# Kernel optimization log

Measured on AMD Instinct MI355X. Metric: run time of the kernel, lower is better.

Reference implementation:

```python
import jax, jax.numpy as jnp
import numpy as np

MARGIN = 0.5
SCALE = 64.0

N, D, C, S = 512, 512, 100000, 1


def setup_inputs() -> dict:
    key = jax.random.key(0)
    k1, k2, k3 = jax.random.split(key, 3)
    emb = jax.random.normal(k1, (N, D), dtype=jnp.float32)
    # Real face pipelines feed L2-normalized embeddings; also keeps acos well-conditioned.
    emb = emb / jnp.linalg.norm(emb, axis=1, keepdims=True)
    w = jax.random.normal(k2, (D, C, S), dtype=jnp.float32)
    labels = jax.random.randint(k3, (N,), 0, C)
    target = jax.nn.one_hot(labels, C, dtype=jnp.float32)  # [N, C]
    return {"embedding_batch": emb, "w_param": w, "target_batch": target}


def reference(embedding_batch, w_param, target_batch):
    # normalize class centers over the embedding dim (dim=0 of w)
    w_n = w_param / jnp.linalg.norm(w_param, axis=0, keepdims=True)  # [D, C, S]
    # cosine similarities via GEMM instead of broadcast mult-reduce: [N, C, S]
    cos = jnp.einsum('nd,dcs->ncs', embedding_batch, w_n)
    cos = jnp.clip(cos, -1.0, 1.0)
    cos = jnp.max(cos, axis=2)                    # best subclass -> [N, C]
    theta = jnp.arccos(cos)                       # [N, C]
    logits = jnp.cos(theta + target_batch * MARGIN) * SCALE
    # faithful to the original: softmax over dim=0 (the batch axis)
    return jax.nn.softmax(logits, axis=0)
```

## Files before the change

### kernel.cpp

```cpp
#include <hip/hip_runtime.h>
#include <hip/hip_bf16.h>


static constexpr int DIM    = 512;
static constexpr int NROWS  = 512;
static constexpr int NCLS   = 100000;
static constexpr int BC     = 32;
static constexpr int BK     = 32;
static constexpr int NSTEP  = DIM / BK;
static constexpr int MT     = NROWS / 16;
static constexpr int NBLK   = NCLS / BC;

static constexpr float COS_M = 0.87758256189037271611f;
static constexpr float SIN_M = 0.47942553860420300027f;
static constexpr float SCALE = 64.0f;
static constexpr float SHIFT = 20.0f;

typedef __attribute__((ext_vector_type(8))) short bf16x8;
typedef __attribute__((ext_vector_type(4))) float f32x4;

#define MFMA16(A, B, C) __builtin_amdgcn_mfma_f32_16x16x32_bf16((A), (B), (C), 0, 0, 0)

__device__ __forceinline__ unsigned short f2bf(float f) {
  union { float f; unsigned u; } v; v.f = f;
  unsigned u = v.u;
  return (unsigned short)((u + 0x7FFFu + ((u >> 16) & 1u)) >> 16);
}

__global__ __launch_bounds__(1024)
void label_scan(const float* __restrict__ tgt, int* __restrict__ labels) {
  const int row = blockIdx.x;
  const int nq = NCLS / 4;
  const int q0 = blockIdx.y * (nq / 4);
  const int q1 = (blockIdx.y == 3) ? nq : q0 + (nq / 4);
  const float4* rp = reinterpret_cast<const float4*>(tgt + (size_t)row * NCLS);
  int found = -1;
  for (int c4 = q0 + threadIdx.x; c4 < q1; c4 += 1024) {
    const float4 v = rp[c4];
    if (v.x > 0.5f) found = c4 * 4 + 0;
    if (v.y > 0.5f) found = c4 * 4 + 1;
    if (v.z > 0.5f) found = c4 * 4 + 2;
    if (v.w > 0.5f) found = c4 * 4 + 3;
  }
  if (found >= 0) labels[row] = found;
}

__global__ void prep_afrag(const float* __restrict__ emb,
                           unsigned short* __restrict__ afrag) {
  const int idx = blockIdx.x * blockDim.x + threadIdx.x;
  const int l  = idx & 63;
  const int mt = (idx >> 6) & 31;
  const int ks = idx >> 11;
  const int row = mt * 16 + (l & 15);
  const int k0  = ks * 32 + (l >> 4) * 8;

  unsigned short t[8];
#pragma unroll
  for (int j = 0; j < 8; ++j) t[j] = f2bf(emb[row * DIM + k0 + j]);

  uint4 v;
  v.x = (unsigned)t[0] | ((unsigned)t[1] << 16);
  v.y = (unsigned)t[2] | ((unsigned)t[3] << 16);
  v.z = (unsigned)t[4] | ((unsigned)t[5] << 16);
  v.w = (unsigned)t[6] | ((unsigned)t[7] << 16);
  *reinterpret_cast<uint4*>(&afrag[(size_t)idx * 8]) = v;
}

__global__ __launch_bounds__(256)
void wt_kernel(const float* __restrict__ w,
               unsigned short* __restrict__ bfrag,
               float* __restrict__ rnorm) {
  __shared__ float S[32][33];
  __shared__ float NRM[32][32];

  const int t  = threadIdx.x;
  const int cb = blockIdx.x;
  const int c0 = cb * 32;

  const int rk = t >> 3;
  const int rc = (t & 7) * 4;

  float4 nrm4 = {0.f, 0.f, 0.f, 0.f};

  for (int p = 0; p < NSTEP; ++p) {
    const float4 v = *reinterpret_cast<const float4*>(
        w + (size_t)(p * BK + rk) * NCLS + c0 + rc);
    nrm4.x += v.x * v.x; nrm4.y += v.y * v.y;
    nrm4.z += v.z * v.z; nrm4.w += v.w * v.w;
    __syncthreads();
    *reinterpret_cast<float4*>(&S[rk][rc]) = v;
    __syncthreads();

    if (t < 128) {
      const int l2 = t & 63;
      const int j  = t >> 6;
      const int col = j * 16 + (l2 & 15);
      const int kb  = (l2 >> 4) * 8;
      uint4 pk;
      pk.x = (unsigned)f2bf(S[kb + 0][col]) | ((unsigned)f2bf(S[kb + 1][col]) << 16);
      pk.y = (unsigned)f2bf(S[kb + 2][col]) | ((unsigned)f2bf(S[kb + 3][col]) << 16);
      pk.z = (unsigned)f2bf(S[kb + 4][col]) | ((unsigned)f2bf(S[kb + 5][col]) << 16);
      pk.w = (unsigned)f2bf(S[kb + 6][col]) | ((unsigned)f2bf(S[kb + 7][col]) << 16);
      *reinterpret_cast<uint4*>(
          &bfrag[(((size_t)(cb * NSTEP + p) * 2 + j) * 64 + l2) * 8]) = pk;
    }
  }

  NRM[rk][rc + 0] = nrm4.x;
  NRM[rk][rc + 1] = nrm4.y;
  NRM[rk][rc + 2] = nrm4.z;
  NRM[rk][rc + 3] = nrm4.w;
  __syncthreads();
  if (t < 32) {
    float s = 0.f;
#pragma unroll
    for (int g = 0; g < 32; ++g) s += NRM[g][t];
    rnorm[c0 + t] = rsqrtf(fmaxf(s, 1e-20f));
  }
}

__global__ __launch_bounds__(1024, 8)
void arcface_main(const unsigned short* __restrict__ bfrag,
                  const unsigned short* __restrict__ afrag,
                  const float* __restrict__ rnorm,
                  const int* __restrict__ labels,
                  float* __restrict__ out) {
  __shared__ alignas(16) unsigned short B3[3][1024];
  __shared__ float red[16][BC];
  __shared__ float colv[BC];

  const int tid = threadIdx.x;
  const int wv  = tid >> 6;
  const int l   = tid & 63;
  const int lh  = l >> 4;
  const int ll  = l & 15;
  const int c0  = blockIdx.x * BC;

  const char* bfb  = (const char*)bfrag + (size_t)blockIdx.x * 32768;
  const char* aptr = (const char*)afrag + (size_t)(wv * 2) * 1024 + (size_t)l * 16;
  char* b3b = (char*)&B3[0][0];

  f32x4 acc[2][2] = {};
  bf16x8 a2[2][2];

#define STAGE(KS, BUF)                                                          \
  if (wv < 2) {                                                                 \
    const int dof = __builtin_amdgcn_readfirstlane((BUF) * 2048 + wv * 1024);   \
    __builtin_amdgcn_global_load_lds(                                           \
        (const __attribute__((address_space(1))) void*)                        \
            (bfb + (size_t)((KS) * 2 + wv) * 1024 + (size_t)l * 16),            \
        (__attribute__((address_space(3))) void*)(b3b + dof), 16, 0, 0);        \
  }

  STAGE(0, 0)
  a2[0][0] = *reinterpret_cast<const bf16x8*>(aptr + 0);
  a2[0][1] = *reinterpret_cast<const bf16x8*>(aptr + 1024);
  STAGE(1, 1)

#define STEP(KS, VMS)                                                           \
  {                                                                             \
    if (wv < 2) { asm volatile("s_waitcnt vmcnt(" #VMS ")" ::: "memory"); }     \
    else        { asm volatile("s_waitcnt vmcnt(0)" ::: "memory"); }            \
    __builtin_amdgcn_s_barrier();                                               \
    __builtin_amdgcn_sched_barrier(0);                                          \
    bf16x8 b0 = *reinterpret_cast<const bf16x8*>(b3b + ((KS) % 3) * 2048 + l * 16);        \
    bf16x8 b1 = *reinterpret_cast<const bf16x8*>(b3b + ((KS) % 3) * 2048 + 1024 + l * 16); \
    if ((KS) + 1 < NSTEP) {                                                     \
      a2[((KS) + 1) & 1][0] =                                                   \
          *reinterpret_cast<const bf16x8*>(aptr + (size_t)((KS) + 1) * 32768);  \
      a2[((KS) + 1) & 1][1] =                                                   \
          *reinterpret_cast<const bf16x8*>(aptr + (size_t)((KS) + 1) * 32768 + 1024); \
    }                                                                           \
    asm volatile("s_waitcnt lgkmcnt(0)" ::: "memory");                          \
    __builtin_amdgcn_sched_barrier(0);                                          \
    if ((KS) + 2 < NSTEP) STAGE((KS) + 2, ((KS) + 2) % 3)                       \
    acc[0][0] = MFMA16(a2[(KS) & 1][0], b0, acc[0][0]);                         \
    acc[0][1] = MFMA16(a2[(KS) & 1][0], b1, acc[0][1]);                         \
    acc[1][0] = MFMA16(a2[(KS) & 1][1], b0, acc[1][0]);                         \
    acc[1][1] = MFMA16(a2[(KS) & 1][1], b1, acc[1][1]);                         \
  }

  STEP(0, 1)   STEP(1, 1)   STEP(2, 1)   STEP(3, 1)
  STEP(4, 1)   STEP(5, 1)   STEP(6, 1)   STEP(7, 1)
  STEP(8, 1)   STEP(9, 1)   STEP(10, 1)  STEP(11, 1)
  STEP(12, 1)  STEP(13, 1)  STEP(14, 1)  STEP(15, 0)
#undef STEP
#undef STAGE

  float rn[2];
#pragma unroll
  for (int j = 0; j < 2; ++j) rn[j] = rnorm[c0 + j * 16 + ll];

  int lab[2][4];
#pragma unroll
  for (int i = 0; i < 2; ++i)
#pragma unroll
    for (int q = 0; q < 4; ++q)
      lab[i][q] = labels[wv * 32 + i * 16 + lh * 4 + q];

  float sme[2] = {0.f, 0.f};
#pragma unroll
  for (int j = 0; j < 2; ++j) {
    const int cj = c0 + j * 16 + ll;
#pragma unroll
    for (int i = 0; i < 2; ++i) {
#pragma unroll
      for (int q = 0; q < 4; ++q) {
        float cosv = acc[i][j][q] * rn[j];
        cosv = fminf(fmaxf(cosv, -1.f), 1.f);
        float lg;
        if (lab[i][q] == cj) {
          const float s = sqrtf(fmaxf(1.f - cosv * cosv, 0.f));
          lg = cosv * COS_M - s * SIN_M;
        } else {
          lg = cosv;
        }
        const float e = __expf(lg * SCALE - SHIFT);
        acc[i][j][q] = e;
        sme[j] += e;
      }
    }
  }

#pragma unroll
  for (int j = 0; j < 2; ++j) {
    sme[j] += __shfl_xor(sme[j], 16, 64);
    sme[j] += __shfl_xor(sme[j], 32, 64);
  }
  __syncthreads();
  if (l < 16) {
#pragma unroll
    for (int j = 0; j < 2; ++j) red[wv][j * 16 + l] = sme[j];
  }
  __syncthreads();
  if (tid < BC) {
    float s = 0.f;
#pragma unroll
    for (int v2 = 0; v2 < 16; ++v2) s += red[v2][tid];
    colv[tid] = s;
  }
  __syncthreads();

  float rs[2];
#pragma unroll
  for (int j = 0; j < 2; ++j) rs[j] = 1.0f / colv[j * 16 + ll];

#pragma unroll
  for (int j = 0; j < 2; ++j) {
    const int cj = c0 + j * 16 + ll;
#pragma unroll
    for (int i = 0; i < 2; ++i) {
#pragma unroll
      for (int q = 0; q < 4; ++q) {
        const int row = wv * 32 + i * 16 + lh * 4 + q;
        out[(size_t)row * NCLS + cj] = acc[i][j][q] * rs[j];
      }
    }
  }
}

extern "C" void kernel_launch(void* const* d_in, const int* in_sizes, int n_in,
                              void* d_out, int out_size, void* d_ws, size_t ws_size,
                              hipStream_t stream) {
  const float* emb = (const float*)d_in[0];
  const float* w   = (const float*)d_in[1];
  const float* tgt = (const float*)d_in[2];
  float* out = (float*)d_out;

  char* ws = (char*)d_ws;
  int* labels           = (int*)ws;
  unsigned short* afrag = (unsigned short*)(ws + 4096);
  float* rnorm          = (float*)(ws + (1u << 20));
  unsigned short* bfrag = (unsigned short*)(ws + (2u << 20));

  label_scan<<<dim3(NROWS, 4), 1024, 0, stream>>>(tgt, labels);
  prep_afrag<<<64, 512, 0, stream>>>(emb, afrag);
  wt_kernel<<<NBLK, 256, 0, stream>>>(w, bfrag, rnorm);
  arcface_main<<<NBLK, 1024, 0, stream>>>(bfrag, afrag, rnorm, labels, out);
}
```

Baseline: 269.0 us.

## Double K-step depth in main GEMM pipeline to halve barriers

Raises the per-iteration K chunk from 32 to 64 in the main kernel, so each pipeline step stages four B fragments via four waves and issues eight MFMAs instead of four, across 8 steps instead of 16. The transpose kernel keeps its 32-wide layout by hardcoding 16 passes, so the fragment memory layout is unchanged. The intent is to halve the barrier and waitcnt stalls per unit of work and give each sync more MFMA work to cover load latency. In exchange it doubles LDS staging per block, holds more A registers, and lowers the launch-bounds occupancy hint from 8 to 4.

```diff
diff --git a/kernel.cpp b/kernel.cpp
--- a/kernel.cpp
+++ b/kernel.cpp
@@ -6,7 +6,7 @@
 static constexpr int NROWS  = 512;
 static constexpr int NCLS   = 100000;
 static constexpr int BC     = 32;
-static constexpr int BK     = 32;
+static constexpr int BK     = 64;
 static constexpr int NSTEP  = DIM / BK;
 static constexpr int MT     = NROWS / 16;
 static constexpr int NBLK   = NCLS / BC;
@@ -82,9 +82,9 @@
 
   float4 nrm4 = {0.f, 0.f, 0.f, 0.f};
 
-  for (int p = 0; p < NSTEP; ++p) {
+  for (int p = 0; p < 16; ++p) {
     const float4 v = *reinterpret_cast<const float4*>(
-        w + (size_t)(p * BK + rk) * NCLS + c0 + rc);
+        w + (size_t)(p * 32 + rk) * NCLS + c0 + rc);
     nrm4.x += v.x * v.x; nrm4.y += v.y * v.y;
     nrm4.z += v.z * v.z; nrm4.w += v.w * v.w;
     __syncthreads();
@@ -102,7 +102,7 @@
       pk.z = (unsigned)f2bf(S[kb + 4][col]) | ((unsigned)f2bf(S[kb + 5][col]) << 16);
       pk.w = (unsigned)f2bf(S[kb + 6][col]) | ((unsigned)f2bf(S[kb + 7][col]) << 16);
       *reinterpret_cast<uint4*>(
-          &bfrag[(((size_t)(cb * NSTEP + p) * 2 + j) * 64 + l2) * 8]) = pk;
+          &bfrag[(((size_t)(cb * 16 + p) * 2 + j) * 64 + l2) * 8]) = pk;
     }
   }
 
@@ -119,13 +119,13 @@
   }
 }
 
-__global__ __launch_bounds__(1024, 8)
+__global__ __launch_bounds__(1024, 4)
 void arcface_main(const unsigned short* __restrict__ bfrag,
                   const unsigned short* __restrict__ afrag,
                   const float* __restrict__ rnorm,
                   const int* __restrict__ labels,
                   float* __restrict__ out) {
-  __shared__ alignas(16) unsigned short B3[3][1024];
+  __shared__ alignas(16) unsigned short B3[3][2048];
   __shared__ float red[16][BC];
   __shared__ float colv[BC];
 
@@ -141,51 +141,58 @@
   char* b3b = (char*)&B3[0][0];
 
   f32x4 acc[2][2] = {};
-  bf16x8 a2[2][2];
+  bf16x8 a2[2][4];
 
 #define STAGE(KS, BUF)                                                          \
-  if (wv < 2) {                                                                 \
-    const int dof = __builtin_amdgcn_readfirstlane((BUF) * 2048 + wv * 1024);   \
+  if (wv < 4) {                                                                 \
+    const int dof = __builtin_amdgcn_readfirstlane((BUF) * 4096 + wv * 1024);   \
     __builtin_amdgcn_global_load_lds(                                           \
         (const __attribute__((address_space(1))) void*)                        \
-            (bfb + (size_t)((KS) * 2 + wv) * 1024 + (size_t)l * 16),            \
+            (bfb + (size_t)((KS) * 4 + wv) * 1024 + (size_t)l * 16),            \
         (__attribute__((address_space(3))) void*)(b3b + dof), 16, 0, 0);        \
   }
 
+#define LOADA(KS, RING)                                                         \
+  {                                                                             \
+    a2[RING][0] = *reinterpret_cast<const bf16x8*>(aptr + (size_t)(2 * (KS) + 0) * 32768);          \
+    a2[RING][1] = *reinterpret_cast<const bf16x8*>(aptr + (size_t)(2 * (KS) + 0) * 32768 + 1024);   \
+    a2[RING][2] = *reinterpret_cast<const bf16x8*>(aptr + (size_t)(2 * (KS) + 1) * 32768);          \
+    a2[RING][3] = *reinterpret_cast<const bf16x8*>(aptr + (size_t)(2 * (KS) + 1) * 32768 + 1024);   \
+  }
+
   STAGE(0, 0)
-  a2[0][0] = *reinterpret_cast<const bf16x8*>(aptr + 0);
-  a2[0][1] = *reinterpret_cast<const bf16x8*>(aptr + 1024);
+  LOADA(0, 0)
   STAGE(1, 1)
 
 #define STEP(KS, VMS)                                                           \
   {                                                                             \
-    if (wv < 2) { asm volatile("s_waitcnt vmcnt(" #VMS ")" ::: "memory"); }     \
+    if (wv < 4) { asm volatile("s_waitcnt vmcnt(" #VMS ")" ::: "memory"); }     \
     else        { asm volatile("s_waitcnt vmcnt(0)" ::: "memory"); }            \
     __builtin_amdgcn_s_barrier();                                               \
     __builtin_amdgcn_sched_barrier(0);                                          \
-    bf16x8 b0 = *reinterpret_cast<const bf16x8*>(b3b + ((KS) % 3) * 2048 + l * 16);        \
-    bf16x8 b1 = *reinterpret_cast<const bf16x8*>(b3b + ((KS) % 3) * 2048 + 1024 + l * 16); \
-    if ((KS) + 1 < NSTEP) {                                                     \
-      a2[((KS) + 1) & 1][0] =                                                   \
-          *reinterpret_cast<const bf16x8*>(aptr + (size_t)((KS) + 1) * 32768);  \
-      a2[((KS) + 1) & 1][1] =                                                   \
-          *reinterpret_cast<const bf16x8*>(aptr + (size_t)((KS) + 1) * 32768 + 1024); \
-    }                                                                           \
+    bf16x8 b00 = *reinterpret_cast<const bf16x8*>(b3b + ((KS) % 3) * 4096 + 0 * 1024 + l * 16); \
+    bf16x8 b01 = *reinterpret_cast<const bf16x8*>(b3b + ((KS) % 3) * 4096 + 1 * 1024 + l * 16); \
+    bf16x8 b10 = *reinterpret_cast<const bf16x8*>(b3b + ((KS) % 3) * 4096 + 2 * 1024 + l * 16); \
+    bf16x8 b11 = *reinterpret_cast<const bf16x8*>(b3b + ((KS) % 3) * 4096 + 3 * 1024 + l * 16); \
+    if ((KS) + 1 < NSTEP) LOADA((KS) + 1, ((KS) + 1) & 1)                       \
     asm volatile("s_waitcnt lgkmcnt(0)" ::: "memory");                          \
     __builtin_amdgcn_sched_barrier(0);                                          \
     if ((KS) + 2 < NSTEP) STAGE((KS) + 2, ((KS) + 2) % 3)                       \
-    acc[0][0] = MFMA16(a2[(KS) & 1][0], b0, acc[0][0]);                         \
-    acc[0][1] = MFMA16(a2[(KS) & 1][0], b1, acc[0][1]);                         \
-    acc[1][0] = MFMA16(a2[(KS) & 1][1], b0, acc[1][0]);                         \
-    acc[1][1] = MFMA16(a2[(KS) & 1][1], b1, acc[1][1]);                         \
-  }
-
-  STEP(0, 1)   STEP(1, 1)   STEP(2, 1)   STEP(3, 1)
-  STEP(4, 1)   STEP(5, 1)   STEP(6, 1)   STEP(7, 1)
-  STEP(8, 1)   STEP(9, 1)   STEP(10, 1)  STEP(11, 1)
-  STEP(12, 1)  STEP(13, 1)  STEP(14, 1)  STEP(15, 0)
+    acc[0][0] = MFMA16(a2[(KS) & 1][0], b00, acc[0][0]);                        \
+    acc[0][1] = MFMA16(a2[(KS) & 1][0], b01, acc[0][1]);                        \
+    acc[1][0] = MFMA16(a2[(KS) & 1][1], b00, acc[1][0]);                        \
+    acc[1][1] = MFMA16(a2[(KS) & 1][1], b01, acc[1][1]);                        \
+    acc[0][0] = MFMA16(a2[(KS) & 1][2], b10, acc[0][0]);                        \
+    acc[0][1] = MFMA16(a2[(KS) & 1][2], b11, acc[0][1]);                        \
+    acc[1][0] = MFMA16(a2[(KS) & 1][3], b10, acc[1][0]);                        \
+    acc[1][1] = MFMA16(a2[(KS) & 1][3], b11, acc[1][1]);                        \
+  }
+
+  STEP(0, 1)  STEP(1, 1)  STEP(2, 1)  STEP(3, 1)
+  STEP(4, 1)  STEP(5, 1)  STEP(6, 1)  STEP(7, 0)
 #undef STEP
 #undef STAGE
+#undef LOADA
 
   float rn[2];
 #pragma unroll
```

Result: slower. 289.9 us (+7.8%).
